# Kernel optimization log

Hardware: AMD Instinct MI355X
Metric: run time of the kernel (lower is better)

Reference implementation:

```python
import jax, jax.numpy as jnp
import numpy as np
from jax import lax

N_LAYER = 4
D_MODEL = 512
N_HEAD = 8
D_HEAD = 64
D_INNER = 2048
KERNEL = 9
POOL = 8
N_CLASSES = 10
BATCH = 4
RAW_LEN = 8192


def setup_inputs() -> dict:
    key = jax.random.key(0)
    ks = jax.random.split(key, 12)
    s = 0.02
    return {
        "signal": jax.random.normal(ks[0], (BATCH, RAW_LEN), jnp.float32),
        "conv_w": jax.random.normal(ks[1], (KERNEL, 1, D_MODEL), jnp.float32) * s,
        "conv_b": jnp.zeros((D_MODEL,), jnp.float32),
        "qkv_w": jax.random.normal(ks[2], (N_LAYER, D_MODEL, 3 * N_HEAD * D_HEAD), jnp.float32) * s,
        "r_w": jax.random.normal(ks[3], (N_LAYER, D_MODEL, N_HEAD * D_HEAD), jnp.float32) * s,
        "o_w": jax.random.normal(ks[4], (N_LAYER, N_HEAD * D_HEAD, D_MODEL), jnp.float32) * s,
        "ff1_w": jax.random.normal(ks[5], (N_LAYER, D_MODEL, D_INNER), jnp.float32) * s,
        "ff1_b": jnp.zeros((N_LAYER, D_INNER), jnp.float32),
        "ff2_w": jax.random.normal(ks[6], (N_LAYER, D_INNER, D_MODEL), jnp.float32) * s,
        "ff2_b": jnp.zeros((N_LAYER, D_MODEL), jnp.float32),
        "r_w_bias": jax.random.normal(ks[7], (N_HEAD, D_HEAD), jnp.float32) * s,
        "r_r_bias": jax.random.normal(ks[8], (N_HEAD, D_HEAD), jnp.float32) * s,
        "fc_w": jax.random.normal(ks[9], (D_MODEL, N_CLASSES), jnp.float32) * s,
        "fc_b": jnp.zeros((N_CLASSES,), jnp.float32),
    }


def _rel_shift(x):
    # x: [qlen, rlen, bsz, n_head]; TF-XL pad/reshape/slice trick
    q, r, b, n = x.shape
    x = jnp.pad(x, ((0, 0), (1, 0), (0, 0), (0, 0)))
    x = x.reshape(r + 1, q, b, n)[1:]
    return x.reshape(q, r, b, n)


def _forward(signal, conv_w, conv_b, qkv_w, r_w, o_w, ff1_w, ff1_b, ff2_w,
             ff2_b, r_w_bias, r_r_bias, fc_w, fc_b):
    # Conv1D (valid) -> ReLU -> AveragePooling1D
    x = signal[:, :, None]  # [B, L, 1]
    x = lax.conv_general_dilated(x, conv_w, (1,), 'VALID',
                                 dimension_numbers=('NWC', 'WIO', 'NWC')) + conv_b
    x = jax.nn.relu(x)
    B, Lp, D = x.shape
    S = Lp // POOL  # Lp is divisible by POOL for our sizes (keras valid pooling)
    x = x[:, :S * POOL].reshape(B, S, POOL, D).mean(axis=2)
    core = x.transpose(1, 0, 2)  # [S, B, D]

    # sinusoidal relative positional embedding, pos_seq = S-1 .. -(S-1)
    pos_seq = jnp.arange(S - 1, -S, -1, dtype=core.dtype)  # [2S-1]
    inv_freq = 1.0 / (10000.0 ** (jnp.arange(0, D, 2, dtype=core.dtype) / D))
    sin_inp = pos_seq[:, None] * inv_freq[None, :]
    pos_emb = jnp.concatenate([jnp.sin(sin_inp), jnp.cos(sin_inp)], -1)  # [2S-1, D]

    scale = 1.0 / np.sqrt(D_HEAD).astype(np.float32)
    for l in range(N_LAYER):
        heads = core @ qkv_w[l]  # [S, B, 3*H*Dh]
        q, k, v = jnp.split(heads, 3, axis=-1)
        q = q.reshape(S, B, N_HEAD, D_HEAD)
        k = k.reshape(S, B, N_HEAD, D_HEAD)
        v = v.reshape(S, B, N_HEAD, D_HEAD)
        rk = (pos_emb @ r_w[l]).reshape(2 * S - 1, N_HEAD, D_HEAD)

        AC = jnp.einsum('ibnd,jbnd->ijbn', q + r_w_bias, k)      # content term
        BD = jnp.einsum('ibnd,jnd->ijbn', q + r_r_bias, rk)      # position term
        BD = _rel_shift(BD)[:, :S]                                # [S, S, B, H]
        attn_prob = jax.nn.softmax((AC + BD) * scale, axis=1)
        attn_vec = jnp.einsum('ijbn,jbnd->ibnd', attn_prob, v)
        attn_out = attn_vec.reshape(S, B, N_HEAD * D_HEAD) @ o_w[l]
        core = core + attn_out

        # position-wise FF with residual
        h = jax.nn.relu(core @ ff1_w[l] + ff1_b[l]) @ ff2_w[l] + ff2_b[l]
        core = core + h

    # classification head on last timestep
    return core[-1] @ fc_w + fc_b  # [B, n_classes]


def reference(signal, conv_w, conv_b, qkv_w, r_w, o_w, ff1_w, ff1_b, ff2_w,
              ff2_b, r_w_bias, r_r_bias, fc_w, fc_b):
    return _forward(signal, conv_w, conv_b, qkv_w, r_w, o_w, ff1_w, ff1_b,
                    ff2_w, ff2_b, r_w_bias, r_r_bias, fc_w, fc_b)
```

## Files before the change

kernel.cpp:

```cpp
#include <hip/hip_runtime.h>
#include <math.h>

#define S_LEN   1023
#define BATCH_N 4
#define DMODEL  512
#define NHEAD   8
#define DHEAD   64
#define DINNER  2048
#define NLAYER  4
#define RAWLEN  8192
#define POOLW   8
#define KERNW   9
#define RLEN    (2*S_LEN-1)
#define MROWS   (S_LEN*BATCH_N)

using bf16x8 = __attribute__((ext_vector_type(8))) short;
using f32x4  = __attribute__((ext_vector_type(4))) float;

__device__ __forceinline__ unsigned short f2bf(float f) {
    union { float f; unsigned int u; } v; v.f = f;
    unsigned int u = v.u;
    return (unsigned short)((u + 0x7fffu + ((u >> 16) & 1u)) >> 16);
}
__device__ __forceinline__ float bf2f(unsigned short h) {
    union { unsigned int u; float f; } v; v.u = ((unsigned int)h) << 16;
    return v.f;
}

__device__ __forceinline__ void gload_lds16(const void* g, void* l) {
    using gvoid = const __attribute__((address_space(1))) void;
    using lvoid = __attribute__((address_space(3))) void;
    gvoid* gp = reinterpret_cast<gvoid*>(reinterpret_cast<unsigned long long>(g));
    lvoid* lp = reinterpret_cast<lvoid*>((unsigned int)reinterpret_cast<unsigned long long>(l));
    __builtin_amdgcn_global_load_lds(gp, lp, 16, 0, 0);
}

__global__ __launch_bounds__(512) void conv_pool_kernel(
    const float* __restrict__ sig, const float* __restrict__ cw,
    const float* __restrict__ cb, float* __restrict__ core,
    unsigned short* __restrict__ core_bf)
{
    int s = blockIdx.x, b = blockIdx.y, d = threadIdx.x;
    __shared__ float sseg[POOLW + KERNW - 1];
    if (d < POOLW + KERNW - 1) sseg[d] = sig[b*RAWLEN + s*POOLW + d];
    __syncthreads();
    float w[KERNW];
#pragma unroll
    for (int k = 0; k < KERNW; k++) w[k] = cw[k*DMODEL + d];
    float bias = cb[d];
    float acc = 0.f;
#pragma unroll
    for (int p = 0; p < POOLW; p++) {
        float c = bias;
#pragma unroll
        for (int k = 0; k < KERNW; k++) c = fmaf(sseg[p+k], w[k], c);
        acc += fmaxf(c, 0.f);
    }
    float v = acc * (1.0f/POOLW);
    core[(s*BATCH_N + b)*DMODEL + d] = v;
    core_bf[(s*BATCH_N + b)*DMODEL + d] = f2bf(v);
}

__global__ __launch_bounds__(512) void posemb_kernel(unsigned short* __restrict__ pe)
{
    int j = blockIdx.x, d = threadIdx.x;
    float pos = (float)(S_LEN - 1 - j);
    int i = (d < 256) ? d : d - 256;
    float invf = powf(10000.0f, -(float)i * (1.0f/256.0f));
    float a = pos * invf;
    pe[j*DMODEL + d] = f2bf((d < 256) ? sinf(a) : cosf(a));
}

__global__ __launch_bounds__(256) void transpose_cvt_kernel(
    const float* __restrict__ W, unsigned short* __restrict__ Wt, int K, int N)
{
    __shared__ float L[32][33];
    int n0 = blockIdx.x*32, k0 = blockIdx.y*32;
    int t = threadIdx.x;
    int kk = t>>3, nq = (t&7)*4;
    float4 v = *reinterpret_cast<const float4*>(&W[(size_t)(k0+kk)*N + n0 + nq]);
    L[kk][nq+0]=v.x; L[kk][nq+1]=v.y; L[kk][nq+2]=v.z; L[kk][nq+3]=v.w;
    __syncthreads();
    int nn = t>>3, kq = (t&7)*4;
    ushort4 o;
    o.x = f2bf(L[kq+0][nn]); o.y = f2bf(L[kq+1][nn]);
    o.z = f2bf(L[kq+2][nn]); o.w = f2bf(L[kq+3][nn]);
    *reinterpret_cast<ushort4*>(&Wt[(size_t)(n0+nn)*K + k0 + kq]) = o;
}

template<int BN, bool ACCUM, bool BIAS, bool RELU, bool WF32, bool WBF>
__global__ __launch_bounds__(256) void gemm_mfma(
    const unsigned short* __restrict__ A, const unsigned short* __restrict__ Bt,
    const float* __restrict__ bias, float* __restrict__ C,
    unsigned short* __restrict__ Cb, int M, int N, int K)
{
    constexpr int MF = (BN == 128) ? 4 : 2;
    __shared__ unsigned short As[128*32];
    __shared__ unsigned short Bs[BN*32];
    int bm = blockIdx.y * 128, bn = blockIdx.x * BN;
    int tid = threadIdx.x, lane = tid & 63, wid = tid >> 6;

    f32x4 acc[MF][4];
#pragma unroll
    for (int m=0;m<MF;m++)
#pragma unroll
        for (int n=0;n<4;n++) acc[m][n] = (f32x4){0.f,0.f,0.f,0.f};

    int r0 = wid*16 + (lane>>2);
    int slot = (lane&3)*8;
    int ga0 = bm + r0;      if (ga0 > M-1) ga0 = M-1;
    int ga1 = bm + r0 + 64; if (ga1 > M-1) ga1 = M-1;
    const unsigned short* pA0 = A  + (size_t)ga0*K + slot;
    const unsigned short* pA1 = A  + (size_t)ga1*K + slot;
    const unsigned short* pB0 = Bt + (size_t)(bn + r0)*K + slot;
    const unsigned short* pB1 = (BN==128) ? Bt + (size_t)(bn + r0 + 64)*K + slot : nullptr;
    char* lA0 = (char*)As + wid*1024;
    char* lA1 = (char*)As + (wid+4)*1024;
    char* lB0 = (char*)Bs + wid*1024;
    char* lB1 = (char*)Bs + (wid+4)*1024;

    int ar = (BN==128 ? (wid>>1)*64 : wid*32) + (lane&15);
    int br = (BN==128 ? (wid&1)*64 : 0) + (lane&15);
    int kc = (lane>>4)*8;

    for (int k0 = 0; k0 < K; k0 += 32) {
        __syncthreads();
        gload_lds16(pA0, lA0);
        gload_lds16(pA1, lA1);
        gload_lds16(pB0, lB0);
        if (BN == 128) gload_lds16(pB1, lB1);
        pA0 += 32; pA1 += 32; pB0 += 32; if (BN==128) pB1 += 32;
        __syncthreads();
        bf16x8 a[MF], b[4];
#pragma unroll
        for (int m=0;m<MF;m++) a[m] = *reinterpret_cast<const bf16x8*>(&As[(ar + m*16)*32 + kc]);
#pragma unroll
        for (int n=0;n<4;n++) b[n] = *reinterpret_cast<const bf16x8*>(&Bs[(br + n*16)*32 + kc]);
#pragma unroll
        for (int m=0;m<MF;m++)
#pragma unroll
            for (int n=0;n<4;n++)
                acc[m][n] = __builtin_amdgcn_mfma_f32_16x16x32_bf16(a[m], b[n], acc[m][n], 0,0,0);
    }

    int col0 = bn + (BN==128 ? (wid&1)*64 : 0) + (lane&15);
    int rbase = bm + (BN==128 ? (wid>>1)*64 : wid*32) + (lane>>4)*4;
#pragma unroll
    for (int m=0;m<MF;m++) {
#pragma unroll
        for (int n=0;n<4;n++) {
            int col = col0 + n*16;
            float bv = BIAS ? bias[col] : 0.f;
#pragma unroll
            for (int r=0;r<4;r++) {
                int row = rbase + m*16 + r;
                if (row < M) {
                    float v = acc[m][n][r] + bv;
                    if (RELU) v = fmaxf(v, 0.f);
                    size_t off = (size_t)row*N + col;
                    if (ACCUM) v += C[off];
                    if (WF32) C[off] = v;
                    if (WBF)  Cb[off] = f2bf(v);
                }
            }
        }
    }
}

#define TI 32
#define TJ 32
#define PSTR 40
#define ACSTR 36
#define BDSTR 68

__global__ __launch_bounds__(256) void attn_mfma_kernel(
    const unsigned short* __restrict__ heads,
    const unsigned short* __restrict__ rk,
    const float* __restrict__ rwb, const float* __restrict__ rrb,
    unsigned short* __restrict__ av)
{
    int i0 = blockIdx.x * TI;
    int bn = blockIdx.y; int b = bn >> 3, n = bn & 7;
    int tid = threadIdx.x, lane = tid & 63, wid = tid >> 6;
    int mi = wid >> 1;
    int half = wid & 1;
    int kc = (lane>>4)*8;
    int l15 = lane & 15;

    __shared__ float Sac[TI*ACSTR];
    __shared__ float Sbd[TI*BDSTR];
    __shared__ unsigned short Pb[TI*PSTR];
    __shared__ float mrow[TI], lrow[TI], frow[TI];

    const int base0 = (S_LEN-1) - i0 - (TI-1);

    bf16x8 qwf0, qwf1, qrf0, qrf1;
    {
        int gi = i0 + mi*16 + l15; if (gi > S_LEN-1) gi = S_LEN-1;
        const unsigned short* qb = heads + (size_t)(gi*BATCH_N + b)*1536 + n*64;
        bf16x8 u0 = *reinterpret_cast<const bf16x8*>(qb + kc);
        bf16x8 u1 = *reinterpret_cast<const bf16x8*>(qb + 32 + kc);
#pragma unroll
        for (int e=0;e<8;e++) {
            float f0 = bf2f((unsigned short)u0[e]);
            float f1 = bf2f((unsigned short)u1[e]);
            qwf0[e] = (short)f2bf(f0 + rwb[n*64 + kc + e]);
            qrf0[e] = (short)f2bf(f0 + rrb[n*64 + kc + e]);
            qwf1[e] = (short)f2bf(f1 + rwb[n*64 + 32 + kc + e]);
            qrf1[e] = (short)f2bf(f1 + rrb[n*64 + 32 + kc + e]);
        }
    }
    if (tid < TI) { mrow[tid] = -1e30f; lrow[tid] = 0.f; }

    f32x4 Oa[2];
    Oa[0] = (f32x4){0.f,0.f,0.f,0.f};
    Oa[1] = (f32x4){0.f,0.f,0.f,0.f};

    int rw = mi*16 + (lane>>4)*4;

    for (int t = 0; t < 32; t++) {
        int j0 = t * TJ;
        __syncthreads();

        {
            int gj = j0 + half*16 + l15; if (gj > S_LEN-1) gj = S_LEN-1;
            const unsigned short* kb = heads + (size_t)(gj*BATCH_N + b)*1536 + 512 + n*64;
            bf16x8 kf0 = *reinterpret_cast<const bf16x8*>(kb + kc);
            bf16x8 kf1 = *reinterpret_cast<const bf16x8*>(kb + 32 + kc);
            f32x4 s = (f32x4){0.f,0.f,0.f,0.f};
            s = __builtin_amdgcn_mfma_f32_16x16x32_bf16(qwf0, kf0, s, 0,0,0);
            s = __builtin_amdgcn_mfma_f32_16x16x32_bf16(qwf1, kf1, s, 0,0,0);
            int ci = half*16 + l15;
#pragma unroll
            for (int r=0;r<4;r++) Sac[(rw+r)*ACSTR + ci] = s[r];
        }
        if (t == 0) {
#pragma unroll
            for (int nn=0;nn<2;nn++) {
                int w = (half*2+nn)*16 + l15;
                int gr = base0 + w; gr = gr < 0 ? 0 : (gr > RLEN-1 ? RLEN-1 : gr);
                const unsigned short* rb = rk + (size_t)gr*DMODEL + n*64;
                bf16x8 rf0 = *reinterpret_cast<const bf16x8*>(rb + kc);
                bf16x8 rf1 = *reinterpret_cast<const bf16x8*>(rb + 32 + kc);
                f32x4 sb = (f32x4){0.f,0.f,0.f,0.f};
                sb = __builtin_amdgcn_mfma_f32_16x16x32_bf16(qrf0, rf0, sb, 0,0,0);
                sb = __builtin_amdgcn_mfma_f32_16x16x32_bf16(qrf1, rf1, sb, 0,0,0);
#pragma unroll
                for (int r=0;r<4;r++) Sbd[(rw+r)*BDSTR + w] = sb[r];
            }
        } else {
            int pblk = ((t & 1) ? 0 : 2) + half;
            int w = pblk*16 + l15;
            int off = 32*(t+1) + (w & 31);
            int gr = base0 + off; gr = gr < 0 ? 0 : (gr > RLEN-1 ? RLEN-1 : gr);
            const unsigned short* rb = rk + (size_t)gr*DMODEL + n*64;
            bf16x8 rf0 = *reinterpret_cast<const bf16x8*>(rb + kc);
            bf16x8 rf1 = *reinterpret_cast<const bf16x8*>(rb + 32 + kc);
            f32x4 sb = (f32x4){0.f,0.f,0.f,0.f};
            sb = __builtin_amdgcn_mfma_f32_16x16x32_bf16(qrf0, rf0, sb, 0,0,0);
            sb = __builtin_amdgcn_mfma_f32_16x16x32_bf16(qrf1, rf1, sb, 0,0,0);
#pragma unroll
            for (int r=0;r<4;r++) Sbd[(rw+r)*BDSTR + w] = sb[r];
        }
        __syncthreads();

        {
            int r = tid>>3, seg = tid&7, jl = seg*4;
            float4 ac = *reinterpret_cast<const float4*>(&Sac[r*ACSTR + jl]);
            int cbase = 32*t + (TI-1) - r;
            float s0 = (ac.x + Sbd[r*BDSTR + ((cbase+jl+0)&63)]) * 0.125f;
            float s1 = (ac.y + Sbd[r*BDSTR + ((cbase+jl+1)&63)]) * 0.125f;
            float s2 = (ac.z + Sbd[r*BDSTR + ((cbase+jl+2)&63)]) * 0.125f;
            float s3 = (ac.w + Sbd[r*BDSTR + ((cbase+jl+3)&63)]) * 0.125f;
            int jg = j0 + jl;
            if (jg+0 >= S_LEN) s0 = -1e30f;
            if (jg+1 >= S_LEN) s1 = -1e30f;
            if (jg+2 >= S_LEN) s2 = -1e30f;
            if (jg+3 >= S_LEN) s3 = -1e30f;
            float tm = fmaxf(fmaxf(s0,s1), fmaxf(s2,s3));
            tm = fmaxf(tm, __shfl_xor(tm, 1));
            tm = fmaxf(tm, __shfl_xor(tm, 2));
            tm = fmaxf(tm, __shfl_xor(tm, 4));
            float mo = mrow[r];
            float mnew = fmaxf(mo, tm);
            float f = __expf(mo - mnew);
            float e0 = __expf(s0 - mnew), e1 = __expf(s1 - mnew);
            float e2 = __expf(s2 - mnew), e3 = __expf(s3 - mnew);
            float ssum = e0+e1+e2+e3;
            ssum += __shfl_xor(ssum, 1);
            ssum += __shfl_xor(ssum, 2);
            ssum += __shfl_xor(ssum, 4);
            if (seg == 0) {
                mrow[r] = mnew;
                lrow[r] = lrow[r]*f + ssum;
                frow[r] = f;
            }
            ushort4 pw;
            pw.x = f2bf(e0); pw.y = f2bf(e1); pw.z = f2bf(e2); pw.w = f2bf(e3);
            *reinterpret_cast<ushort4*>(&Pb[r*PSTR + jl]) = pw;
        }
        __syncthreads();

        {
            float f0 = frow[rw+0], f1 = frow[rw+1], f2 = frow[rw+2], f3 = frow[rw+3];
#pragma unroll
            for (int nn=0;nn<2;nn++) {
                Oa[nn][0] *= f0; Oa[nn][1] *= f1; Oa[nn][2] *= f2; Oa[nn][3] *= f3;
            }
            bf16x8 pf = *reinterpret_cast<const bf16x8*>(&Pb[(mi*16 + l15)*PSTR + kc]);
            const unsigned short* vb = heads + 1024 + n*64;
#pragma unroll
            for (int nn=0;nn<2;nn++) {
                int d = (half*2+nn)*16 + l15;
                bf16x8 vf;
#pragma unroll
                for (int e=0;e<8;e++) {
                    int gj = j0 + kc + e; if (gj > S_LEN-1) gj = S_LEN-1;
                    vf[e] = (short)vb[(size_t)(gj*BATCH_N + b)*1536 + d];
                }
                Oa[nn] = __builtin_amdgcn_mfma_f32_16x16x32_bf16(pf, vf, Oa[nn], 0,0,0);
            }
        }
    }
    __syncthreads();

    {
        float linv[4];
#pragma unroll
        for (int r=0;r<4;r++) linv[r] = 1.0f / lrow[rw+r];
#pragma unroll
        for (int nn=0;nn<2;nn++) {
            int d = (half*2+nn)*16 + l15;
#pragma unroll
            for (int r=0;r<4;r++) {
                int gi = i0 + rw + r;
                if (gi < S_LEN)
                    av[(size_t)(gi*BATCH_N + b)*DMODEL + n*64 + d] = f2bf(Oa[nn][r]*linv[r]);
            }
        }
    }
}

__global__ __launch_bounds__(64) void final_kernel(
    const float* __restrict__ core, const float* __restrict__ fcw,
    const float* __restrict__ fcb, float* __restrict__ out)
{
    int idx = blockIdx.x;
    int b = idx / 10, c = idx % 10;
    int lane = threadIdx.x;
    const float* row = &core[(size_t)((S_LEN-1)*BATCH_N + b)*DMODEL];
    float acc = 0.f;
    for (int d = lane; d < DMODEL; d += 64)
        acc = fmaf(row[d], fcw[d*10 + c], acc);
#pragma unroll
    for (int off = 32; off; off >>= 1) acc += __shfl_xor(acc, off);
    if (lane == 0) out[b*10 + c] = acc + fcb[c];
}

extern "C" void kernel_launch(void* const* d_in, const int* in_sizes, int n_in,
                              void* d_out, int out_size, void* d_ws, size_t ws_size,
                              hipStream_t stream)
{
    const float* sig   = (const float*)d_in[0];
    const float* cw    = (const float*)d_in[1];
    const float* cb    = (const float*)d_in[2];
    const float* qkv_w = (const float*)d_in[3];
    const float* r_w   = (const float*)d_in[4];
    const float* o_w   = (const float*)d_in[5];
    const float* ff1_w = (const float*)d_in[6];
    const float* ff1_b = (const float*)d_in[7];
    const float* ff2_w = (const float*)d_in[8];
    const float* ff2_b = (const float*)d_in[9];
    const float* rwb   = (const float*)d_in[10];
    const float* rrb   = (const float*)d_in[11];
    const float* fcw   = (const float*)d_in[12];
    const float* fcb   = (const float*)d_in[13];
    float* out = (float*)d_out;

    float* core = (float*)d_ws;
    unsigned short* core_bf = (unsigned short*)(core + (size_t)MROWS*DMODEL);
    unsigned short* pe_bf   = core_bf + (size_t)MROWS*DMODEL;
    unsigned short* rk_bf   = pe_bf   + (size_t)RLEN*DMODEL;
    unsigned short* av_bf   = rk_bf   + (size_t)RLEN*DMODEL;
    unsigned short* big_bf  = av_bf   + (size_t)MROWS*DMODEL;
    unsigned short* qkvT = big_bf + (size_t)MROWS*DINNER;
    unsigned short* rwT  = qkvT + (size_t)(3*DMODEL)*DMODEL;
    unsigned short* owT  = rwT  + (size_t)DMODEL*DMODEL;
    unsigned short* ff1T = owT  + (size_t)DMODEL*DMODEL;
    unsigned short* ff2T = ff1T + (size_t)DINNER*DMODEL;

    conv_pool_kernel<<<dim3(S_LEN, BATCH_N), 512, 0, stream>>>(sig, cw, cb, core, core_bf);
    posemb_kernel<<<RLEN, 512, 0, stream>>>(pe_bf);

    for (int l = 0; l < NLAYER; l++) {
        transpose_cvt_kernel<<<dim3(48,16), 256, 0, stream>>>(
            qkv_w + (size_t)l*DMODEL*(3*DMODEL), qkvT, DMODEL, 3*DMODEL);
        transpose_cvt_kernel<<<dim3(16,16), 256, 0, stream>>>(
            r_w + (size_t)l*DMODEL*DMODEL, rwT, DMODEL, DMODEL);
        transpose_cvt_kernel<<<dim3(16,16), 256, 0, stream>>>(
            o_w + (size_t)l*DMODEL*DMODEL, owT, DMODEL, DMODEL);
        transpose_cvt_kernel<<<dim3(64,16), 256, 0, stream>>>(
            ff1_w + (size_t)l*DMODEL*DINNER, ff1T, DMODEL, DINNER);
        transpose_cvt_kernel<<<dim3(16,64), 256, 0, stream>>>(
            ff2_w + (size_t)l*DINNER*DMODEL, ff2T, DINNER, DMODEL);

        gemm_mfma<128,false,false,false,false,true><<<dim3(12,32), 256, 0, stream>>>(
            core_bf, qkvT, nullptr, nullptr, big_bf, MROWS, 3*DMODEL, DMODEL);
        gemm_mfma<64,false,false,false,false,true><<<dim3(8,16), 256, 0, stream>>>(
            pe_bf, rwT, nullptr, nullptr, rk_bf, RLEN, DMODEL, DMODEL);
        attn_mfma_kernel<<<dim3(32,32), 256, 0, stream>>>(big_bf, rk_bf, rwb, rrb, av_bf);
        gemm_mfma<64,true,false,false,true,true><<<dim3(8,32), 256, 0, stream>>>(
            av_bf, owT, nullptr, core, core_bf, MROWS, DMODEL, DMODEL);
        gemm_mfma<128,false,true,true,false,true><<<dim3(16,32), 256, 0, stream>>>(
            core_bf, ff1T, ff1_b + (size_t)l*DINNER, nullptr, big_bf, MROWS, DINNER, DMODEL);
        gemm_mfma<64,true,true,false,true,true><<<dim3(8,32), 256, 0, stream>>>(
            big_bf, ff2T, ff2_b + (size_t)l*DMODEL, core, core_bf, MROWS, DMODEL, DINNER);
    }

    final_kernel<<<40, 64, 0, stream>>>(core, fcw, fcb, out);
}
```

Before: 843.2 us.

## Fuse weight transposes, add 64x64 GEMM tile, split attention waves by term

Merges the five per-layer weight transpose launches into one kernel, adds a smaller 64x64-tile MFMA GEMM for the N=512 projections so they launch more blocks, and switches the QKV GEMM to the 64-wide tile. The attention kernel moves to 512 threads, with separate waves for the content and position score terms and one output tile per wave. The positional embedding uses exp2f and fast sin/cos. Together these aim to cut launch overhead and raise occupancy on small GEMMs and attention, at the cost of less reuse per tile and slightly less precise positional values.

```diff
diff --git a/kernel.cpp b/kernel.cpp
--- a/kernel.cpp
+++ b/kernel.cpp
@@ -66,16 +66,29 @@
     int j = blockIdx.x, d = threadIdx.x;
     float pos = (float)(S_LEN - 1 - j);
     int i = (d < 256) ? d : d - 256;
-    float invf = powf(10000.0f, -(float)i * (1.0f/256.0f));
+    float invf = exp2f(-(float)i * (13.287712f/256.0f));
     float a = pos * invf;
-    pe[j*DMODEL + d] = f2bf((d < 256) ? sinf(a) : cosf(a));
-}
-
-__global__ __launch_bounds__(256) void transpose_cvt_kernel(
-    const float* __restrict__ W, unsigned short* __restrict__ Wt, int K, int N)
-{
+    pe[j*DMODEL + d] = f2bf((d < 256) ? __sinf(a) : __cosf(a));
+}
+
+__global__ __launch_bounds__(256) void transpose_all_kernel(
+    const float* __restrict__ qw, const float* __restrict__ rw,
+    const float* __restrict__ ow, const float* __restrict__ f1,
+    const float* __restrict__ f2,
+    unsigned short* __restrict__ qT, unsigned short* __restrict__ rT,
+    unsigned short* __restrict__ oT, unsigned short* __restrict__ f1T,
+    unsigned short* __restrict__ f2T)
+{
+    int id = blockIdx.x;
+    const float* W; unsigned short* Wt; int K, N, bx, by;
+    if (id < 768)       { W = qw;  Wt = qT;  K = 512;  N = 1536; bx = id % 48; by = id / 48; }
+    else if (id < 1024) { id -= 768;  W = rw;  Wt = rT;  K = 512;  N = 512;  bx = id % 16; by = id / 16; }
+    else if (id < 1280) { id -= 1024; W = ow;  Wt = oT;  K = 512;  N = 512;  bx = id % 16; by = id / 16; }
+    else if (id < 2304) { id -= 1280; W = f1;  Wt = f1T; K = 512;  N = 2048; bx = id % 64; by = id / 64; }
+    else                { id -= 2304; W = f2;  Wt = f2T; K = 2048; N = 512;  bx = id % 16; by = id / 16; }
+
     __shared__ float L[32][33];
-    int n0 = blockIdx.x*32, k0 = blockIdx.y*32;
+    int n0 = bx*32, k0 = by*32;
     int t = threadIdx.x;
     int kk = t>>3, nq = (t&7)*4;
     float4 v = *reinterpret_cast<const float4*>(&W[(size_t)(k0+kk)*N + n0 + nq]);
@@ -167,13 +180,85 @@
     }
 }
 
+template<bool ACCUM, bool BIAS, bool RELU, bool WF32, bool WBF>
+__global__ __launch_bounds__(256) void gemm_mfma64(
+    const unsigned short* __restrict__ A, const unsigned short* __restrict__ Bt,
+    const float* __restrict__ bias, float* __restrict__ C,
+    unsigned short* __restrict__ Cb, int M, int N, int K)
+{
+    __shared__ unsigned short As[64*32];
+    __shared__ unsigned short Bs[64*32];
+    int bm = blockIdx.y * 64, bn = blockIdx.x * 64;
+    int tid = threadIdx.x, lane = tid & 63, wid = tid >> 6;
+    int wr = wid >> 1, wc = wid & 1;
+
+    f32x4 acc[2][2];
+#pragma unroll
+    for (int m=0;m<2;m++)
+#pragma unroll
+        for (int n=0;n<2;n++) acc[m][n] = (f32x4){0.f,0.f,0.f,0.f};
+
+    int r0 = wid*16 + (lane>>2);
+    int slot = (lane&3)*8;
+    int ga = bm + r0; if (ga > M-1) ga = M-1;
+    const unsigned short* pA = A  + (size_t)ga*K + slot;
+    const unsigned short* pB = Bt + (size_t)(bn + r0)*K + slot;
+    char* lA = (char*)As + wid*1024;
+    char* lB = (char*)Bs + wid*1024;
+
+    int ar = wr*32 + (lane&15);
+    int br = wc*32 + (lane&15);
+    int kc = (lane>>4)*8;
+
+    for (int k0 = 0; k0 < K; k0 += 32) {
+        __syncthreads();
+        gload_lds16(pA, lA);
+        gload_lds16(pB, lB);
+        pA += 32; pB += 32;
+        __syncthreads();
+        bf16x8 a[2], b[2];
+#pragma unroll
+        for (int m=0;m<2;m++) a[m] = *reinterpret_cast<const bf16x8*>(&As[(ar + m*16)*32 + kc]);
+#pragma unroll
+        for (int n=0;n<2;n++) b[n] = *reinterpret_cast<const bf16x8*>(&Bs[(br + n*16)*32 + kc]);
+#pragma unroll
+        for (int m=0;m<2;m++)
+#pragma unroll
+            for (int n=0;n<2;n++)
+                acc[m][n] = __builtin_amdgcn_mfma_f32_16x16x32_bf16(a[m], b[n], acc[m][n], 0,0,0);
+    }
+
+    int col0 = bn + wc*32 + (lane&15);
+    int rbase = bm + wr*32 + (lane>>4)*4;
+#pragma unroll
+    for (int m=0;m<2;m++) {
+#pragma unroll
+        for (int n=0;n<2;n++) {
+            int col = col0 + n*16;
+            float bv = BIAS ? bias[col] : 0.f;
+#pragma unroll
+            for (int r=0;r<4;r++) {
+                int row = rbase + m*16 + r;
+                if (row < M) {
+                    float v = acc[m][n][r] + bv;
+                    if (RELU) v = fmaxf(v, 0.f);
+                    size_t off = (size_t)row*N + col;
+                    if (ACCUM) v += C[off];
+                    if (WF32) C[off] = v;
+                    if (WBF)  Cb[off] = f2bf(v);
+                }
+            }
+        }
+    }
+}
+
 #define TI 32
 #define TJ 32
 #define PSTR 40
 #define ACSTR 36
 #define BDSTR 68
 
-__global__ __launch_bounds__(256) void attn_mfma_kernel(
+__global__ __launch_bounds__(512) void attn_mfma_kernel(
     const unsigned short* __restrict__ heads,
     const unsigned short* __restrict__ rk,
     const float* __restrict__ rwb, const float* __restrict__ rrb,
@@ -182,10 +267,8 @@
     int i0 = blockIdx.x * TI;
     int bn = blockIdx.y; int b = bn >> 3, n = bn & 7;
     int tid = threadIdx.x, lane = tid & 63, wid = tid >> 6;
-    int mi = wid >> 1;
-    int half = wid & 1;
+    int l15 = lane & 15;
     int kc = (lane>>4)*8;
-    int l15 = lane & 15;
 
     __shared__ float Sac[TI*ACSTR];
     __shared__ float Sbd[TI*BDSTR];
@@ -194,59 +277,58 @@
 
     const int base0 = (S_LEN-1) - i0 - (TI-1);
 
-    bf16x8 qwf0, qwf1, qrf0, qrf1;
+    bool isAC = wid < 4;
+    int mi = isAC ? (wid>>1) : ((wid-4)>>1);
+    int half = wid & 1;
+
+    bf16x8 qa0, qa1;
     {
         int gi = i0 + mi*16 + l15; if (gi > S_LEN-1) gi = S_LEN-1;
         const unsigned short* qb = heads + (size_t)(gi*BATCH_N + b)*1536 + n*64;
+        const float* qbias = isAC ? rwb : rrb;
         bf16x8 u0 = *reinterpret_cast<const bf16x8*>(qb + kc);
         bf16x8 u1 = *reinterpret_cast<const bf16x8*>(qb + 32 + kc);
 #pragma unroll
         for (int e=0;e<8;e++) {
-            float f0 = bf2f((unsigned short)u0[e]);
-            float f1 = bf2f((unsigned short)u1[e]);
-            qwf0[e] = (short)f2bf(f0 + rwb[n*64 + kc + e]);
-            qrf0[e] = (short)f2bf(f0 + rrb[n*64 + kc + e]);
-            qwf1[e] = (short)f2bf(f1 + rwb[n*64 + 32 + kc + e]);
-            qrf1[e] = (short)f2bf(f1 + rrb[n*64 + 32 + kc + e]);
+            qa0[e] = (short)f2bf(bf2f((unsigned short)u0[e]) + qbias[n*64 + kc + e]);
+            qa1[e] = (short)f2bf(bf2f((unsigned short)u1[e]) + qbias[n*64 + 32 + kc + e]);
         }
     }
     if (tid < TI) { mrow[tid] = -1e30f; lrow[tid] = 0.f; }
 
-    f32x4 Oa[2];
-    Oa[0] = (f32x4){0.f,0.f,0.f,0.f};
-    Oa[1] = (f32x4){0.f,0.f,0.f,0.f};
-
-    int rw = mi*16 + (lane>>4)*4;
+    int pmi = wid >> 2, pdblk = wid & 3;
+    int rwq = mi*16 + (lane>>4)*4;
+    int rwp = pmi*16 + (lane>>4)*4;
+    f32x4 Oa = (f32x4){0.f,0.f,0.f,0.f};
 
     for (int t = 0; t < 32; t++) {
         int j0 = t * TJ;
         __syncthreads();
 
-        {
+        if (isAC) {
             int gj = j0 + half*16 + l15; if (gj > S_LEN-1) gj = S_LEN-1;
             const unsigned short* kb = heads + (size_t)(gj*BATCH_N + b)*1536 + 512 + n*64;
             bf16x8 kf0 = *reinterpret_cast<const bf16x8*>(kb + kc);
             bf16x8 kf1 = *reinterpret_cast<const bf16x8*>(kb + 32 + kc);
             f32x4 s = (f32x4){0.f,0.f,0.f,0.f};
-            s = __builtin_amdgcn_mfma_f32_16x16x32_bf16(qwf0, kf0, s, 0,0,0);
-            s = __builtin_amdgcn_mfma_f32_16x16x32_bf16(qwf1, kf1, s, 0,0,0);
+            s = __builtin_amdgcn_mfma_f32_16x16x32_bf16(qa0, kf0, s, 0,0,0);
+            s = __builtin_amdgcn_mfma_f32_16x16x32_bf16(qa1, kf1, s, 0,0,0);
             int ci = half*16 + l15;
 #pragma unroll
-            for (int r=0;r<4;r++) Sac[(rw+r)*ACSTR + ci] = s[r];
-        }
-        if (t == 0) {
-#pragma unroll
-            for (int nn=0;nn<2;nn++) {
-                int w = (half*2+nn)*16 + l15;
+            for (int r=0;r<4;r++) Sac[(rwq+r)*ACSTR + ci] = s[r];
+        } else if (t == 0) {
+#pragma unroll
+            for (int q=0;q<2;q++) {
+                int w = (half + q*2)*16 + l15;
                 int gr = base0 + w; gr = gr < 0 ? 0 : (gr > RLEN-1 ? RLEN-1 : gr);
                 const unsigned short* rb = rk + (size_t)gr*DMODEL + n*64;
                 bf16x8 rf0 = *reinterpret_cast<const bf16x8*>(rb + kc);
                 bf16x8 rf1 = *reinterpret_cast<const bf16x8*>(rb + 32 + kc);
                 f32x4 sb = (f32x4){0.f,0.f,0.f,0.f};
-                sb = __builtin_amdgcn_mfma_f32_16x16x32_bf16(qrf0, rf0, sb, 0,0,0);
-                sb = __builtin_amdgcn_mfma_f32_16x16x32_bf16(qrf1, rf1, sb, 0,0,0);
-#pragma unroll
-                for (int r=0;r<4;r++) Sbd[(rw+r)*BDSTR + w] = sb[r];
+                sb = __builtin_amdgcn_mfma_f32_16x16x32_bf16(qa0, rf0, sb, 0,0,0);
+                sb = __builtin_amdgcn_mfma_f32_16x16x32_bf16(qa1, rf1, sb, 0,0,0);
+#pragma unroll
+                for (int r=0;r<4;r++) Sbd[(rwq+r)*BDSTR + w] = sb[r];
             }
         } else {
             int pblk = ((t & 1) ? 0 : 2) + half;
@@ -257,85 +339,71 @@
             bf16x8 rf0 = *reinterpret_cast<const bf16x8*>(rb + kc);
             bf16x8 rf1 = *reinterpret_cast<const bf16x8*>(rb + 32 + kc);
             f32x4 sb = (f32x4){0.f,0.f,0.f,0.f};
-            sb = __builtin_amdgcn_mfma_f32_16x16x32_bf16(qrf0, rf0, sb, 0,0,0);
-            sb = __builtin_amdgcn_mfma_f32_16x16x32_bf16(qrf1, rf1, sb, 0,0,0);
-#pragma unroll
-            for (int r=0;r<4;r++) Sbd[(rw+r)*BDSTR + w] = sb[r];
+            sb = __builtin_amdgcn_mfma_f32_16x16x32_bf16(qa0, rf0, sb, 0,0,0);
+            sb = __builtin_amdgcn_mfma_f32_16x16x32_bf16(qa1, rf1, sb, 0,0,0);
+#pragma unroll
+            for (int r=0;r<4;r++) Sbd[(rwq+r)*BDSTR + w] = sb[r];
         }
         __syncthreads();
 
         {
-            int r = tid>>3, seg = tid&7, jl = seg*4;
-            float4 ac = *reinterpret_cast<const float4*>(&Sac[r*ACSTR + jl]);
-            int cbase = 32*t + (TI-1) - r;
-            float s0 = (ac.x + Sbd[r*BDSTR + ((cbase+jl+0)&63)]) * 0.125f;
-            float s1 = (ac.y + Sbd[r*BDSTR + ((cbase+jl+1)&63)]) * 0.125f;
-            float s2 = (ac.z + Sbd[r*BDSTR + ((cbase+jl+2)&63)]) * 0.125f;
-            float s3 = (ac.w + Sbd[r*BDSTR + ((cbase+jl+3)&63)]) * 0.125f;
+            int r = tid >> 4, sg = tid & 15, jl = sg*2;
+            float a0 = Sac[r*ACSTR + jl], a1 = Sac[r*ACSTR + jl + 1];
+            int cb2 = 32*t + (TI-1) - r;
+            float s0 = (a0 + Sbd[r*BDSTR + ((cb2+jl  )&63)]) * 0.125f;
+            float s1 = (a1 + Sbd[r*BDSTR + ((cb2+jl+1)&63)]) * 0.125f;
             int jg = j0 + jl;
             if (jg+0 >= S_LEN) s0 = -1e30f;
             if (jg+1 >= S_LEN) s1 = -1e30f;
-            if (jg+2 >= S_LEN) s2 = -1e30f;
-            if (jg+3 >= S_LEN) s3 = -1e30f;
-            float tm = fmaxf(fmaxf(s0,s1), fmaxf(s2,s3));
+            float tm = fmaxf(s0, s1);
             tm = fmaxf(tm, __shfl_xor(tm, 1));
             tm = fmaxf(tm, __shfl_xor(tm, 2));
             tm = fmaxf(tm, __shfl_xor(tm, 4));
+            tm = fmaxf(tm, __shfl_xor(tm, 8));
             float mo = mrow[r];
             float mnew = fmaxf(mo, tm);
             float f = __expf(mo - mnew);
             float e0 = __expf(s0 - mnew), e1 = __expf(s1 - mnew);
-            float e2 = __expf(s2 - mnew), e3 = __expf(s3 - mnew);
-            float ssum = e0+e1+e2+e3;
+            float ssum = e0 + e1;
             ssum += __shfl_xor(ssum, 1);
             ssum += __shfl_xor(ssum, 2);
             ssum += __shfl_xor(ssum, 4);
-            if (seg == 0) {
+            ssum += __shfl_xor(ssum, 8);
+            if (sg == 0) {
                 mrow[r] = mnew;
                 lrow[r] = lrow[r]*f + ssum;
                 frow[r] = f;
             }
-            ushort4 pw;
-            pw.x = f2bf(e0); pw.y = f2bf(e1); pw.z = f2bf(e2); pw.w = f2bf(e3);
-            *reinterpret_cast<ushort4*>(&Pb[r*PSTR + jl]) = pw;
+            *reinterpret_cast<ushort2*>(&Pb[r*PSTR + jl]) =
+                make_ushort2(f2bf(e0), f2bf(e1));
         }
         __syncthreads();
 
         {
-            float f0 = frow[rw+0], f1 = frow[rw+1], f2 = frow[rw+2], f3 = frow[rw+3];
-#pragma unroll
-            for (int nn=0;nn<2;nn++) {
-                Oa[nn][0] *= f0; Oa[nn][1] *= f1; Oa[nn][2] *= f2; Oa[nn][3] *= f3;
-            }
-            bf16x8 pf = *reinterpret_cast<const bf16x8*>(&Pb[(mi*16 + l15)*PSTR + kc]);
-            const unsigned short* vb = heads + 1024 + n*64;
-#pragma unroll
-            for (int nn=0;nn<2;nn++) {
-                int d = (half*2+nn)*16 + l15;
-                bf16x8 vf;
-#pragma unroll
-                for (int e=0;e<8;e++) {
-                    int gj = j0 + kc + e; if (gj > S_LEN-1) gj = S_LEN-1;
-                    vf[e] = (short)vb[(size_t)(gj*BATCH_N + b)*1536 + d];
-                }
-                Oa[nn] = __builtin_amdgcn_mfma_f32_16x16x32_bf16(pf, vf, Oa[nn], 0,0,0);
-            }
+            float f0 = frow[rwp+0], f1 = frow[rwp+1], f2 = frow[rwp+2], f3 = frow[rwp+3];
+            Oa[0] *= f0; Oa[1] *= f1; Oa[2] *= f2; Oa[3] *= f3;
+            bf16x8 pf = *reinterpret_cast<const bf16x8*>(&Pb[(pmi*16 + l15)*PSTR + kc]);
+            int d = pdblk*16 + l15;
+            const unsigned short* vb = heads + 1024 + n*64 + d;
+            bf16x8 vf;
+#pragma unroll
+            for (int e=0;e<8;e++) {
+                int gj = j0 + kc + e; if (gj > S_LEN-1) gj = S_LEN-1;
+                vf[e] = (short)vb[(size_t)(gj*BATCH_N + b)*1536];
+            }
+            Oa = __builtin_amdgcn_mfma_f32_16x16x32_bf16(pf, vf, Oa, 0,0,0);
         }
     }
     __syncthreads();
 
     {
-        float linv[4];
-#pragma unroll
-        for (int r=0;r<4;r++) linv[r] = 1.0f / lrow[rw+r];
-#pragma unroll
-        for (int nn=0;nn<2;nn++) {
-            int d = (half*2+nn)*16 + l15;
-#pragma unroll
-            for (int r=0;r<4;r++) {
-                int gi = i0 + rw + r;
-                if (gi < S_LEN)
-                    av[(size_t)(gi*BATCH_N + b)*DMODEL + n*64 + d] = f2bf(Oa[nn][r]*linv[r]);
+        int d = pdblk*16 + l15;
+#pragma unroll
+        for (int r=0;r<4;r++) {
+            int gi = i0 + rwp + r;
+            if (gi < S_LEN) {
+                float o = Oa[r] / lrow[rwp + r];
+                av[(size_t)(gi*BATCH_N + b)*DMODEL + n*64 + d] = f2bf(o);
             }
         }
     }
@@ -393,27 +461,24 @@
     posemb_kernel<<<RLEN, 512, 0, stream>>>(pe_bf);
 
     for (int l = 0; l < NLAYER; l++) {
-        transpose_cvt_kernel<<<dim3(48,16), 256, 0, stream>>>(
-            qkv_w + (size_t)l*DMODEL*(3*DMODEL), qkvT, DMODEL, 3*DMODEL);
-        transpose_cvt_kernel<<<dim3(16,16), 256, 0, stream>>>(
-            r_w + (size_t)l*DMODEL*DMODEL, rwT, DMODEL, DMODEL);
-        transpose_cvt_kernel<<<dim3(16,16), 256, 0, stream>>>(
-            o_w + (size_t)l*DMODEL*DMODEL, owT, DMODEL, DMODEL);
-        transpose_cvt_kernel<<<dim3(64,16), 256, 0, stream>>>(
-            ff1_w + (size_t)l*DMODEL*DINNER, ff1T, DMODEL, DINNER);
-        transpose_cvt_kernel<<<dim3(16,64), 256, 0, stream>>>(
-            ff2_w + (size_t)l*DINNER*DMODEL, ff2T, DINNER, DMODEL);
-
-        gemm_mfma<128,false,false,false,false,true><<<dim3(12,32), 256, 0, stream>>>(
+        transpose_all_kernel<<<3328, 256, 0, stream>>>(
+            qkv_w + (size_t)l*DMODEL*(3*DMODEL),
+            r_w   + (size_t)l*DMODEL*DMODEL,
+            o_w   + (size_t)l*DMODEL*DMODEL,
+            ff1_w + (size_t)l*DMODEL*DINNER,
+            ff2_w + (size_t)l*DINNER*DMODEL,
+            qkvT, rwT, owT, ff1T, ff2T);
+
+        gemm_mfma<64,false,false,false,false,true><<<dim3(24,32), 256, 0, stream>>>(
             core_bf, qkvT, nullptr, nullptr, big_bf, MROWS, 3*DMODEL, DMODEL);
-        gemm_mfma<64,false,false,false,false,true><<<dim3(8,16), 256, 0, stream>>>(
+        gemm_mfma64<false,false,false,false,true><<<dim3(8,32), 256, 0, stream>>>(
             pe_bf, rwT, nullptr, nullptr, rk_bf, RLEN, DMODEL, DMODEL);
-        attn_mfma_kernel<<<dim3(32,32), 256, 0, stream>>>(big_bf, rk_bf, rwb, rrb, av_bf);
-        gemm_mfma<64,true,false,false,true,true><<<dim3(8,32), 256, 0, stream>>>(
+        attn_mfma_kernel<<<dim3(32,32), 512, 0, stream>>>(big_bf, rk_bf, rwb, rrb, av_bf);
+        gemm_mfma64<true,false,false,true,true><<<dim3(8,64), 256, 0, stream>>>(
             av_bf, owT, nullptr, core, core_bf, MROWS, DMODEL, DMODEL);
         gemm_mfma<128,false,true,true,false,true><<<dim3(16,32), 256, 0, stream>>>(
             core_bf, ff1T, ff1_b + (size_t)l*DINNER, nullptr, big_bf, MROWS, DINNER, DMODEL);
-        gemm_mfma<64,true,true,false,true,true><<<dim3(8,32), 256, 0, stream>>>(
+        gemm_mfma64<true,true,false,true,true><<<dim3(8,64), 256, 0, stream>>>(
             big_bf, ff2T, ff2_b + (size_t)l*DMODEL, core, core_bf, MROWS, DMODEL, DINNER);
     }
 
```

Result: slower. 875.9 us (+3.9%).

## Merge weight transposes, add 64x64 GEMM tile, use fast posemb math

Applied to the files above, without the earlier changes.

Merges the five per-layer weight transpose launches into one kernel that dispatches on block index. Adds a 64x64-tile MFMA GEMM, used for the r_w, o_w and ff2 projections, and switches the QKV GEMM to the 64-wide tile, so these small-N GEMMs launch more blocks and fill more compute units. The positional embedding now uses exp2f and the fast __sinf/__cosf intrinsics, which risks small precision differences at large arguments. Smaller tiles give up some data reuse per block in exchange for parallelism.

```diff
diff --git a/kernel.cpp b/kernel.cpp
--- a/kernel.cpp
+++ b/kernel.cpp
@@ -66,16 +66,29 @@
     int j = blockIdx.x, d = threadIdx.x;
     float pos = (float)(S_LEN - 1 - j);
     int i = (d < 256) ? d : d - 256;
-    float invf = powf(10000.0f, -(float)i * (1.0f/256.0f));
+    float invf = exp2f(-(float)i * (13.287712f/256.0f));
     float a = pos * invf;
-    pe[j*DMODEL + d] = f2bf((d < 256) ? sinf(a) : cosf(a));
-}
-
-__global__ __launch_bounds__(256) void transpose_cvt_kernel(
-    const float* __restrict__ W, unsigned short* __restrict__ Wt, int K, int N)
-{
+    pe[j*DMODEL + d] = f2bf((d < 256) ? __sinf(a) : __cosf(a));
+}
+
+__global__ __launch_bounds__(256) void transpose_all_kernel(
+    const float* __restrict__ qw, const float* __restrict__ rw,
+    const float* __restrict__ ow, const float* __restrict__ f1,
+    const float* __restrict__ f2,
+    unsigned short* __restrict__ qT, unsigned short* __restrict__ rT,
+    unsigned short* __restrict__ oT, unsigned short* __restrict__ f1T,
+    unsigned short* __restrict__ f2T)
+{
+    int id = blockIdx.x;
+    const float* W; unsigned short* Wt; int K, N, bx, by;
+    if (id < 768)       { W = qw;  Wt = qT;  K = 512;  N = 1536; bx = id % 48; by = id / 48; }
+    else if (id < 1024) { id -= 768;  W = rw;  Wt = rT;  K = 512;  N = 512;  bx = id % 16; by = id / 16; }
+    else if (id < 1280) { id -= 1024; W = ow;  Wt = oT;  K = 512;  N = 512;  bx = id % 16; by = id / 16; }
+    else if (id < 2304) { id -= 1280; W = f1;  Wt = f1T; K = 512;  N = 2048; bx = id % 64; by = id / 64; }
+    else                { id -= 2304; W = f2;  Wt = f2T; K = 2048; N = 512;  bx = id % 16; by = id / 16; }
+
     __shared__ float L[32][33];
-    int n0 = blockIdx.x*32, k0 = blockIdx.y*32;
+    int n0 = bx*32, k0 = by*32;
     int t = threadIdx.x;
     int kk = t>>3, nq = (t&7)*4;
     float4 v = *reinterpret_cast<const float4*>(&W[(size_t)(k0+kk)*N + n0 + nq]);
@@ -149,6 +162,78 @@
     for (int m=0;m<MF;m++) {
 #pragma unroll
         for (int n=0;n<4;n++) {
+            int col = col0 + n*16;
+            float bv = BIAS ? bias[col] : 0.f;
+#pragma unroll
+            for (int r=0;r<4;r++) {
+                int row = rbase + m*16 + r;
+                if (row < M) {
+                    float v = acc[m][n][r] + bv;
+                    if (RELU) v = fmaxf(v, 0.f);
+                    size_t off = (size_t)row*N + col;
+                    if (ACCUM) v += C[off];
+                    if (WF32) C[off] = v;
+                    if (WBF)  Cb[off] = f2bf(v);
+                }
+            }
+        }
+    }
+}
+
+template<bool ACCUM, bool BIAS, bool RELU, bool WF32, bool WBF>
+__global__ __launch_bounds__(256) void gemm_mfma64(
+    const unsigned short* __restrict__ A, const unsigned short* __restrict__ Bt,
+    const float* __restrict__ bias, float* __restrict__ C,
+    unsigned short* __restrict__ Cb, int M, int N, int K)
+{
+    __shared__ unsigned short As[64*32];
+    __shared__ unsigned short Bs[64*32];
+    int bm = blockIdx.y * 64, bn = blockIdx.x * 64;
+    int tid = threadIdx.x, lane = tid & 63, wid = tid >> 6;
+    int wr = wid >> 1, wc = wid & 1;
+
+    f32x4 acc[2][2];
+#pragma unroll
+    for (int m=0;m<2;m++)
+#pragma unroll
+        for (int n=0;n<2;n++) acc[m][n] = (f32x4){0.f,0.f,0.f,0.f};
+
+    int r0 = wid*16 + (lane>>2);
+    int slot = (lane&3)*8;
+    int ga = bm + r0; if (ga > M-1) ga = M-1;
+    const unsigned short* pA = A  + (size_t)ga*K + slot;
+    const unsigned short* pB = Bt + (size_t)(bn + r0)*K + slot;
+    char* lA = (char*)As + wid*1024;
+    char* lB = (char*)Bs + wid*1024;
+
+    int ar = wr*32 + (lane&15);
+    int br = wc*32 + (lane&15);
+    int kc = (lane>>4)*8;
+
+    for (int k0 = 0; k0 < K; k0 += 32) {
+        __syncthreads();
+        gload_lds16(pA, lA);
+        gload_lds16(pB, lB);
+        pA += 32; pB += 32;
+        __syncthreads();
+        bf16x8 a[2], b[2];
+#pragma unroll
+        for (int m=0;m<2;m++) a[m] = *reinterpret_cast<const bf16x8*>(&As[(ar + m*16)*32 + kc]);
+#pragma unroll
+        for (int n=0;n<2;n++) b[n] = *reinterpret_cast<const bf16x8*>(&Bs[(br + n*16)*32 + kc]);
+#pragma unroll
+        for (int m=0;m<2;m++)
+#pragma unroll
+            for (int n=0;n<2;n++)
+                acc[m][n] = __builtin_amdgcn_mfma_f32_16x16x32_bf16(a[m], b[n], acc[m][n], 0,0,0);
+    }
+
+    int col0 = bn + wc*32 + (lane&15);
+    int rbase = bm + wr*32 + (lane>>4)*4;
+#pragma unroll
+    for (int m=0;m<2;m++) {
+#pragma unroll
+        for (int n=0;n<2;n++) {
             int col = col0 + n*16;
             float bv = BIAS ? bias[col] : 0.f;
 #pragma unroll
@@ -393,27 +478,24 @@
     posemb_kernel<<<RLEN, 512, 0, stream>>>(pe_bf);
 
     for (int l = 0; l < NLAYER; l++) {
-        transpose_cvt_kernel<<<dim3(48,16), 256, 0, stream>>>(
-            qkv_w + (size_t)l*DMODEL*(3*DMODEL), qkvT, DMODEL, 3*DMODEL);
-        transpose_cvt_kernel<<<dim3(16,16), 256, 0, stream>>>(
-            r_w + (size_t)l*DMODEL*DMODEL, rwT, DMODEL, DMODEL);
-        transpose_cvt_kernel<<<dim3(16,16), 256, 0, stream>>>(
-            o_w + (size_t)l*DMODEL*DMODEL, owT, DMODEL, DMODEL);
-        transpose_cvt_kernel<<<dim3(64,16), 256, 0, stream>>>(
-            ff1_w + (size_t)l*DMODEL*DINNER, ff1T, DMODEL, DINNER);
-        transpose_cvt_kernel<<<dim3(16,64), 256, 0, stream>>>(
-            ff2_w + (size_t)l*DINNER*DMODEL, ff2T, DINNER, DMODEL);
-
-        gemm_mfma<128,false,false,false,false,true><<<dim3(12,32), 256, 0, stream>>>(
+        transpose_all_kernel<<<3328, 256, 0, stream>>>(
+            qkv_w + (size_t)l*DMODEL*(3*DMODEL),
+            r_w   + (size_t)l*DMODEL*DMODEL,
+            o_w   + (size_t)l*DMODEL*DMODEL,
+            ff1_w + (size_t)l*DMODEL*DINNER,
+            ff2_w + (size_t)l*DINNER*DMODEL,
+            qkvT, rwT, owT, ff1T, ff2T);
+
+        gemm_mfma<64,false,false,false,false,true><<<dim3(24,32), 256, 0, stream>>>(
             core_bf, qkvT, nullptr, nullptr, big_bf, MROWS, 3*DMODEL, DMODEL);
-        gemm_mfma<64,false,false,false,false,true><<<dim3(8,16), 256, 0, stream>>>(
+        gemm_mfma64<false,false,false,false,true><<<dim3(8,32), 256, 0, stream>>>(
             pe_bf, rwT, nullptr, nullptr, rk_bf, RLEN, DMODEL, DMODEL);
         attn_mfma_kernel<<<dim3(32,32), 256, 0, stream>>>(big_bf, rk_bf, rwb, rrb, av_bf);
-        gemm_mfma<64,true,false,false,true,true><<<dim3(8,32), 256, 0, stream>>>(
+        gemm_mfma64<true,false,false,true,true><<<dim3(8,64), 256, 0, stream>>>(
             av_bf, owT, nullptr, core, core_bf, MROWS, DMODEL, DMODEL);
         gemm_mfma<128,false,true,true,false,true><<<dim3(16,32), 256, 0, stream>>>(
             core_bf, ff1T, ff1_b + (size_t)l*DINNER, nullptr, big_bf, MROWS, DINNER, DMODEL);
-        gemm_mfma<64,true,true,false,true,true><<<dim3(8,32), 256, 0, stream>>>(
+        gemm_mfma64<true,true,false,true,true><<<dim3(8,64), 256, 0, stream>>>(
             big_bf, ff2T, ff2_b + (size_t)l*DMODEL, core, core_bf, MROWS, DMODEL, DINNER);
     }
 
```

After: 729.6 us. 1.16x faster.
